# Kernel optimization log

Measured on AMD Instinct MI355X. Metric: run time of the kernel, lower is better.

## Reference

```python
import jax, jax.numpy as jnp
import numpy as np

EPS = 1e-6  # NAFNet LayerNorm2d eps


def conv1x1(x, W, b):
    # x: [B,C,H,W], W: [O,C], b: [O]
    return jnp.einsum('bchw,oc->bohw', x, W) + b[None, :, None, None]


def layernorm2d(x, w, b):
    # normalize over channel dim (NAFNet LayerNorm2d)
    mu = jnp.mean(x, axis=1, keepdims=True)
    var = jnp.var(x, axis=1, keepdims=True)
    xn = (x - mu) * jax.lax.rsqrt(var + EPS)
    return xn * w[None, :, None, None] + b[None, :, None, None]


def resize_bilinear_ac(x, H, W):
    # bilinear resize with align_corners=True; x: [B,C,h,w] -> [B,C,H,W]
    B, C, h, w = x.shape

    def coords(out, inn):
        s = (inn - 1) / (out - 1)
        c = jnp.arange(out, dtype=jnp.float32) * jnp.float32(s)
        i0 = jnp.clip(jnp.floor(c).astype(jnp.int32), 0, inn - 2)
        f = c - i0.astype(jnp.float32)
        return i0, f

    i0, fy = coords(H, h)
    j0, fx = coords(W, w)
    # rows
    x = x[:, :, i0, :] * (1.0 - fy)[None, None, :, None] + x[:, :, i0 + 1, :] * fy[None, None, :, None]
    # cols
    x = x[:, :, :, j0] * (1.0 - fx)[None, None, None, :] + x[:, :, :, j0 + 1] * fx[None, None, None, :]
    return x


def setup_inputs() -> dict:
    key = jax.random.key(0)
    ks = jax.random.split(key, 24)
    B, c, mem_c, H, W = 8, 128, 64, 128, 128
    h2, w2 = 64, 64
    std = 0.02

    def w2d(k, o, i):
        return jax.random.normal(k, (o, i), dtype=jnp.float32) * np.sqrt(2.0 / o)

    return {
        'x_l': jax.random.normal(ks[0], (B, c, H, W), dtype=jnp.float32),
        'x_r': jax.random.normal(ks[1], (B, mem_c, h2, w2), dtype=jnp.float32),
        'Wm': w2d(ks[2], c, mem_c), 'bm': jnp.zeros((c,), jnp.float32),
        'nl_w': jnp.ones((c,), jnp.float32), 'nl_b': jnp.zeros((c,), jnp.float32),
        'nr_w': jnp.ones((c,), jnp.float32), 'nr_b': jnp.zeros((c,), jnp.float32),
        'Wl1': w2d(ks[3], c, c), 'bl1': jnp.zeros((c,), jnp.float32),
        'Wr1': w2d(ks[4], c, c), 'br1': jnp.zeros((c,), jnp.float32),
        'Wl2': w2d(ks[5], c, c), 'bl2': jnp.zeros((c,), jnp.float32),
        'Wr2': w2d(ks[6], c, c), 'br2': jnp.zeros((c,), jnp.float32),
        'beta': jax.random.normal(ks[7], (1, c, 1, 1), dtype=jnp.float32) * std,
        'gamma': jax.random.normal(ks[8], (1, c, 1, 1), dtype=jnp.float32) * std,
        'Wf': w2d(ks[9], c, 2 * c), 'bf': jnp.zeros((c,), jnp.float32),
    }


def reference(x_l, x_r, Wm, bm, nl_w, nl_b, nr_w, nr_b, Wl1, bl1, Wr1, br1,
              Wl2, bl2, Wr2, br2, beta, gamma, Wf, bf):
    c = x_l.shape[1]
    scale = jnp.float32(c) ** -0.5
    H, W = x_l.shape[-2], x_l.shape[-1]

    x_r = conv1x1(x_r, Wm, bm)
    x_r = resize_bilinear_ac(x_r, H, W)

    Q_l = jnp.transpose(conv1x1(layernorm2d(x_l, nl_w, nl_b), Wl1, bl1), (0, 2, 3, 1))  # b h w c
    Q_r = jnp.transpose(conv1x1(layernorm2d(x_r, nr_w, nr_b), Wr1, br1), (0, 2, 3, 1))  # b h v c
    V_l = jnp.transpose(conv1x1(x_l, Wl2, bl2), (0, 2, 3, 1))  # b h w c
    V_r = jnp.transpose(conv1x1(x_r, Wr2, br2), (0, 2, 3, 1))  # b h v c

    attn = jnp.einsum('bhwc,bhvc->bhwv', Q_l, Q_r) * scale  # [B,H,W,W]
    F_r2l = jnp.einsum('bhwv,bhvc->bhwc', jax.nn.softmax(attn, axis=-1), V_r)
    F_l2r = jnp.einsum('bhwv,bhwc->bhvc', jax.nn.softmax(attn, axis=2), V_l)

    F_r2l = jnp.transpose(F_r2l, (0, 3, 1, 2)) * beta
    F_l2r = jnp.transpose(F_l2r, (0, 3, 1, 2)) * gamma

    x = jnp.concatenate([x_l + F_r2l, x_r + F_l2r], axis=1)
    return conv1x1(x, Wf, bf)
```

## Files before the change

### kernel.cpp

```cpp
#include <hip/hip_runtime.h>
#include <cstdint>
#include <cstddef>

typedef __attribute__((ext_vector_type(8))) short short8;
typedef __attribute__((ext_vector_type(4))) float f32x4;

#define MFMA16(a,b,c) __builtin_amdgcn_mfma_f32_16x16x32_bf16((a),(b),(c),0,0,0)

static __device__ __forceinline__ float bf2f(unsigned short u){
    unsigned int x = ((unsigned int)u) << 16;
    return __builtin_bit_cast(float, x);
}
static __device__ __forceinline__ unsigned short f2bf(float f){
    unsigned int x = __builtin_bit_cast(unsigned int, f);
    x = x + 0x7FFFu + ((x >> 16) & 1u);
    return (unsigned short)(x >> 16);
}


__global__ void k_prep(const float* __restrict__ Wl1, const float* __restrict__ bl1,
                       const float* __restrict__ Wr1, const float* __restrict__ br1,
                       const float* __restrict__ Wl2, const float* __restrict__ Wr2,
                       const float* __restrict__ Wf,
                       const float* __restrict__ nlw, const float* __restrict__ nlb,
                       const float* __restrict__ nrw, const float* __restrict__ nrb,
                       unsigned short* __restrict__ wl1e, unsigned short* __restrict__ wr1e,
                       unsigned short* __restrict__ wl2b, unsigned short* __restrict__ wr2b,
                       unsigned short* __restrict__ wf1b, unsigned short* __restrict__ wf2b,
                       float* __restrict__ S1l, float* __restrict__ S1r,
                       float* __restrict__ beffl, float* __restrict__ beffr)
{
    int o = blockIdx.x;
    int c = threadIdx.x;
    float wl = Wl1[o*128+c] * nlw[c];
    unsigned short wlb = f2bf(wl);
    wl1e[o*128+c] = wlb;
    float wr = Wr1[o*128+c] * nrw[c];
    unsigned short wrb = f2bf(wr);
    wr1e[o*128+c] = wrb;
    wl2b[o*128+c] = f2bf(Wl2[o*128+c]);
    wr2b[o*128+c] = f2bf(Wr2[o*128+c]);
    wf1b[o*128+c] = f2bf(Wf[o*256+c]);
    wf2b[o*128+c] = f2bf(Wf[o*256+128+c]);

    __shared__ float red[4][128];
    red[0][c] = bf2f(wlb);
    red[1][c] = Wl1[o*128+c]*nlb[c];
    red[2][c] = bf2f(wrb);
    red[3][c] = Wr1[o*128+c]*nrb[c];
    __syncthreads();
    if (c < 4) {
        float s = 0.f;
        for (int i = 0; i < 128; i++) s += red[c][i];
        if      (c == 0) S1l[o]   = s;
        else if (c == 1) beffl[o] = bl1[o] + s;
        else if (c == 2) S1r[o]   = s;
        else             beffr[o] = br1[o] + s;
    }
}

__global__ void k_memconv(const float* __restrict__ xr, const float* __restrict__ Wm,
                          const float* __restrict__ bm, unsigned short* __restrict__ R0n)
{
    __shared__ float Xs[64][65];
    __shared__ float Ws[128][65];
    int blk = blockIdx.x;
    int b  = blk >> 6;
    int p0 = (blk & 63) * 64;
    int t = threadIdx.x;
    for (int k = 0; k < 16; k++) {
        int idx = t + 256*k;
        int c = idx >> 6, pi = idx & 63;
        Xs[c][pi] = xr[((long)b*64 + c)*4096 + p0 + pi];
    }
    for (int k = 0; k < 32; k++) {
        int idx = t + 256*k;
        int o = idx >> 6, c = idx & 63;
        Ws[o][c] = Wm[o*64 + c];
    }
    __syncthreads();
    int og = t >> 3, pg = t & 7;
    int o0 = og*4, pp0 = pg*8;
    float acc[4][8];
    #pragma unroll
    for (int j = 0; j < 4; j++)
        #pragma unroll
        for (int k = 0; k < 8; k++) acc[j][k] = bm[o0+j];
    for (int c = 0; c < 64; c++) {
        float xv[8], wv[4];
        #pragma unroll
        for (int k = 0; k < 8; k++) xv[k] = Xs[c][pp0+k];
        #pragma unroll
        for (int j = 0; j < 4; j++) wv[j] = Ws[o0+j][c];
        #pragma unroll
        for (int j = 0; j < 4; j++)
            #pragma unroll
            for (int k = 0; k < 8; k++) acc[j][k] += wv[j]*xv[k];
    }
    #pragma unroll
    for (int j = 0; j < 4; j++)
        #pragma unroll
        for (int k = 0; k < 8; k++)
            R0n[((long)b*4096 + p0 + pp0 + k)*128 + o0 + j] = f2bf(acc[j][k]);
}

__global__ void k_upsample(const unsigned short* __restrict__ R0n,
                           unsigned short* __restrict__ XR)
{
    int t = threadIdx.x;
    int c = t & 127;
    long pix = (long)blockIdx.x * 2 + (t >> 7);
    int b = (int)(pix >> 14);
    int rem = (int)(pix & 16383);
    int Y = rem >> 7, X = rem & 127;
    const float s = 63.0f / 127.0f;
    float cy = Y * s, cx = X * s;
    int y0 = min((int)floorf(cy), 62);
    int x0 = min((int)floorf(cx), 62);
    float fy = cy - (float)y0, fx = cx - (float)x0;
    const unsigned short* base = R0n + ((long)b*4096)*128;
    float v00 = bf2f(base[(y0*64 + x0    )*128 + c]);
    float v01 = bf2f(base[(y0*64 + x0 + 1)*128 + c]);
    float v10 = bf2f(base[((y0+1)*64 + x0    )*128 + c]);
    float v11 = bf2f(base[((y0+1)*64 + x0 + 1)*128 + c]);
    float r0 = v00*(1.f-fy) + v10*fy;
    float r1 = v01*(1.f-fy) + v11*fy;
    XR[pix*128 + c] = f2bf(r0*(1.f-fx) + r1*fx);
}

__global__ void k_transpose(const float* __restrict__ xl, unsigned short* __restrict__ XL)
{
    __shared__ float tile[32][33];
    int blk = blockIdx.x;
    int pt = blk & 511;
    int ct = (blk >> 9) & 3;
    int b  = blk >> 11;
    int p0 = pt*32, c0 = ct*32;
    int t = threadIdx.x;
    const float* src = xl + (long)b*128*16384;
    #pragma unroll
    for (int k = 0; k < 4; k++) {
        int idx = t + 256*k;
        int ci = idx >> 5, pi = idx & 31;
        tile[ci][pi] = src[(long)(c0+ci)*16384 + p0 + pi];
    }
    __syncthreads();
    unsigned short* dst = XL + (long)b*16384*128;
    #pragma unroll
    for (int k = 0; k < 4; k++) {
        int idx = t + 256*k;
        int pi = idx >> 5, ci = idx & 31;
        dst[(long)(p0+pi)*128 + c0 + ci] = f2bf(tile[ci][pi]);
    }
}

__global__ void k_stats(const unsigned short* __restrict__ X,
                        float* __restrict__ mu, float* __restrict__ rs, int npix)
{
    int t = threadIdx.x;
    int lane = t & 63, wv = t >> 6;
    long pix = (long)blockIdx.x*4 + wv;
    if (pix >= npix) return;
    const unsigned short* row = X + pix*128;
    unsigned int pr = *(const unsigned int*)(row + lane*2);
    float a = bf2f((unsigned short)(pr & 0xFFFFu));
    float b = bf2f((unsigned short)(pr >> 16));
    float s = a + b, s2 = a*a + b*b;
    #pragma unroll
    for (int d = 1; d < 64; d <<= 1) { s += __shfl_xor(s, d); s2 += __shfl_xor(s2, d); }
    if (lane == 0) {
        float m = s * (1.0f/128.0f);
        float var = s2 * (1.0f/128.0f) - m*m;
        mu[pix] = m;
        rs[pix] = rsqrtf(var + 1e-6f);
    }
}

#define LDQ 136
constexpr int K4_LDS = 4*128*LDQ*2 + (13*128 + 8*128 + 256)*4;

__global__ __launch_bounds__(512) void k_scam(
    const unsigned short* __restrict__ XL, const unsigned short* __restrict__ XR,
    const unsigned short* __restrict__ wl1e, const unsigned short* __restrict__ wr1e,
    const unsigned short* __restrict__ wl2b, const unsigned short* __restrict__ wr2b,
    const unsigned short* __restrict__ wf1b, const unsigned short* __restrict__ wf2b,
    const float* __restrict__ muL, const float* __restrict__ rsL,
    const float* __restrict__ muR, const float* __restrict__ rsR,
    const float* __restrict__ S1l, const float* __restrict__ S1r,
    const float* __restrict__ beffl, const float* __restrict__ beffr,
    const float* __restrict__ bl2, const float* __restrict__ br2,
    const float* __restrict__ beta, const float* __restrict__ gam,
    const float* __restrict__ bfv, float* __restrict__ out)
{
    extern __shared__ char smem[];
    unsigned short* bufA  = (unsigned short*)smem;
    unsigned short* bufB  = bufA  + 128*LDQ;
    unsigned short* bufVL = bufB  + 128*LDQ;
    unsigned short* bufVR = bufVL + 128*LDQ;
    float* vecs    = (float*)(bufVR + 128*LDQ);
    float* colpart = vecs + 13*128;
    float* colred  = colpart + 8*128;

    int tid = threadIdx.x;
    int lane = tid & 63, wv = tid >> 6;
    int l16 = lane & 15, lg = lane >> 4;
    int bh = blockIdx.x;
    int b = bh >> 7, h = bh & 127;
    long pixbase = (long)b*16384 + (long)h*128;
    const unsigned short* Abl = XL + pixbase*128;
    const unsigned short* Abr = XR + pixbase*128;

    if (tid < 128) {
        vecs[0*128+tid]  = muL[pixbase + tid];
        vecs[1*128+tid]  = rsL[pixbase + tid];
        vecs[2*128+tid]  = muR[pixbase + tid];
        vecs[3*128+tid]  = rsR[pixbase + tid];
        vecs[4*128+tid]  = S1l[tid];
        vecs[5*128+tid]  = beffl[tid];
        vecs[6*128+tid]  = S1r[tid];
        vecs[7*128+tid]  = beffr[tid];
        vecs[8*128+tid]  = bl2[tid];
        vecs[9*128+tid]  = br2[tid];
        vecs[10*128+tid] = beta[tid];
        vecs[11*128+tid] = gam[tid];
        vecs[12*128+tid] = bfv[tid];
    }
    __syncthreads();

    int p0 = wv * 16;

    f32x4 acc[8];
    auto conv = [&](const unsigned short* Asrc, const unsigned short* Wsrc){
        #pragma unroll
        for (int t = 0; t < 8; t++) acc[t] = (f32x4){0.f,0.f,0.f,0.f};
        #pragma unroll
        for (int kc = 0; kc < 4; kc++) {
            short8 a = *(const short8*)(Asrc + (p0+l16)*128 + kc*32 + lg*8);
            #pragma unroll
            for (int t = 0; t < 8; t++) {
                short8 bw = *(const short8*)(Wsrc + (t*16+l16)*128 + kc*32 + lg*8);
                acc[t] = MFMA16(a, bw, acc[t]);
            }
        }
    };
    auto epiQ = [&](const float* vmu, const float* vrs, const float* vS1,
                    const float* vbe, unsigned short* dst){
        #pragma unroll
        for (int r = 0; r < 4; r++) {
            int p = p0 + lg*4 + r;
            float mu = vmu[p], rs = vrs[p];
            #pragma unroll
            for (int t = 0; t < 8; t++) {
                int o = t*16 + l16;
                dst[p*LDQ + o] = f2bf(rs*(acc[t][r] - mu*vS1[o]) + vbe[o]);
            }
        }
    };
    auto epiV = [&](const float* vb, unsigned short* dst){
        #pragma unroll
        for (int t = 0; t < 8; t++) {
            int o = t*16 + l16;
            float bias = vb[o];
            #pragma unroll
            for (int r = 0; r < 4; r++) {
                int p = p0 + lg*4 + r;
                dst[o*LDQ + p] = f2bf(acc[t][r] + bias);
            }
        }
    };

    conv(Abl, wl1e); epiQ(vecs+0*128, vecs+1*128, vecs+4*128, vecs+5*128, bufA);
    conv(Abr, wr1e); epiQ(vecs+2*128, vecs+3*128, vecs+6*128, vecs+7*128, bufB);
    conv(Abl, wl2b); epiV(vecs+8*128, bufVL);
    conv(Abr, wr2b); epiV(vecs+9*128, bufVR);
    __syncthreads();

    int w0 = p0;
    f32x4 s[8];
    #pragma unroll
    for (int t = 0; t < 8; t++) s[t] = (f32x4){0.f,0.f,0.f,0.f};
    #pragma unroll
    for (int kc = 0; kc < 4; kc++) {
        short8 a = *(const short8*)(bufA + (w0+l16)*LDQ + kc*32 + lg*8);
        #pragma unroll
        for (int t = 0; t < 8; t++) {
            short8 bq = *(const short8*)(bufB + (t*16+l16)*LDQ + kc*32 + lg*8);
            s[t] = MFMA16(a, bq, s[t]);
        }
    }
    const float scale = 0.08838834764831845f;
    #pragma unroll
    for (int t = 0; t < 8; t++)
        #pragma unroll
        for (int r = 0; r < 4; r++) s[t][r] *= scale;

    float rm[4];
    #pragma unroll
    for (int r = 0; r < 4; r++) {
        float m = s[0][r];
        #pragma unroll
        for (int t = 1; t < 8; t++) m = fmaxf(m, s[t][r]);
        #pragma unroll
        for (int d = 1; d < 16; d <<= 1) m = fmaxf(m, __shfl_xor(m, d));
        rm[r] = m;
    }
    #pragma unroll
    for (int t = 0; t < 8; t++) {
        float m = fmaxf(fmaxf(s[t][0], s[t][1]), fmaxf(s[t][2], s[t][3]));
        m = fmaxf(m, __shfl_xor(m, 16));
        m = fmaxf(m, __shfl_xor(m, 32));
        if (lane < 16) colpart[wv*128 + t*16 + lane] = m;
    }
    __syncthreads();
    if (tid < 128) {
        float m = colpart[tid];
        for (int i = 1; i < 8; i++) m = fmaxf(m, colpart[i*128 + tid]);
        colred[tid] = m;
    }
    __syncthreads();

    float rsum[4];
    #pragma unroll
    for (int r = 0; r < 4; r++) {
        float a = 0.f;
        #pragma unroll
        for (int t = 0; t < 8; t++) { float e = __expf(s[t][r] - rm[r]); s[t][r] = e; a += e; }
        #pragma unroll
        for (int d = 1; d < 16; d <<= 1) a += __shfl_xor(a, d);
        rsum[r] = a;
    }
    #pragma unroll
    for (int t = 0; t < 8; t++) {
        #pragma unroll
        for (int r = 0; r < 4; r++) {
            bufA[(w0 + lg*4 + r)*LDQ + t*16 + l16] = f2bf(s[t][r] / rsum[r]);
        }
    }
    #pragma unroll
    for (int t = 0; t < 8; t++) {
        float cmax = colred[t*16 + l16];
        float a = 0.f;
        #pragma unroll
        for (int r = 0; r < 4; r++) {
            float e2 = s[t][r] * __expf(rm[r] - cmax);
            s[t][r] = e2; a += e2;
        }
        a += __shfl_xor(a, 16);
        a += __shfl_xor(a, 32);
        if (lane < 16) colpart[wv*128 + t*16 + lane] = a;
    }
    __syncthreads();
    if (tid < 128) {
        float sm = 0.f;
        for (int i = 0; i < 8; i++) sm += colpart[i*128 + tid];
        colred[128 + tid] = sm;
    }
    __syncthreads();
    #pragma unroll
    for (int t = 0; t < 8; t++) {
        float inv = 1.0f / colred[128 + t*16 + l16];
        #pragma unroll
        for (int r = 0; r < 4; r++) {
            bufB[(t*16 + l16)*LDQ + w0 + lg*4 + r] = f2bf(s[t][r] * inv);
        }
    }
    __syncthreads();

    f32x4 f1[8], f2[8];
    #pragma unroll
    for (int t = 0; t < 8; t++) { f1[t] = (f32x4){0.f,0.f,0.f,0.f}; f2[t] = (f32x4){0.f,0.f,0.f,0.f}; }
    #pragma unroll
    for (int kc = 0; kc < 4; kc++) {
        short8 a1 = *(const short8*)(bufA + (w0+l16)*LDQ + kc*32 + lg*8);
        short8 a2 = *(const short8*)(bufB + (w0+l16)*LDQ + kc*32 + lg*8);
        #pragma unroll
        for (int t = 0; t < 8; t++) {
            short8 bv1 = *(const short8*)(bufVR + (t*16+l16)*LDQ + kc*32 + lg*8);
            f1[t] = MFMA16(a1, bv1, f1[t]);
            short8 bv2 = *(const short8*)(bufVL + (t*16+l16)*LDQ + kc*32 + lg*8);
            f2[t] = MFMA16(a2, bv2, f2[t]);
        }
    }
    __syncthreads();

    #pragma unroll
    for (int t = 0; t < 8; t++) {
        int c = t*16 + l16;
        float bet = vecs[10*128 + c], gm = vecs[11*128 + c];
        #pragma unroll
        for (int r = 0; r < 4; r++) {
            int p = w0 + lg*4 + r;
            float xl = bf2f(Abl[p*128 + c]);
            bufA[p*LDQ + c] = f2bf(xl + bet*f1[t][r]);
            float xr = bf2f(Abr[p*128 + c]);
            bufB[p*LDQ + c] = f2bf(xr + gm*f2[t][r]);
        }
    }
    __syncthreads();

    int o0 = wv * 16;
    f32x4 oacc[8];
    #pragma unroll
    for (int t = 0; t < 8; t++) oacc[t] = (f32x4){0.f,0.f,0.f,0.f};
    #pragma unroll
    for (int kc = 0; kc < 4; kc++) {
        short8 aw1 = *(const short8*)(wf1b + (o0+l16)*128 + kc*32 + lg*8);
        short8 aw2 = *(const short8*)(wf2b + (o0+l16)*128 + kc*32 + lg*8);
        #pragma unroll
        for (int t = 0; t < 8; t++) {
            short8 b1 = *(const short8*)(bufA + (t*16+l16)*LDQ + kc*32 + lg*8);
            oacc[t] = MFMA16(aw1, b1, oacc[t]);
            short8 b2 = *(const short8*)(bufB + (t*16+l16)*LDQ + kc*32 + lg*8);
            oacc[t] = MFMA16(aw2, b2, oacc[t]);
        }
    }
    float* outb = out + (long)b*2097152 + (long)h*128;
    #pragma unroll
    for (int t = 0; t < 8; t++) {
        #pragma unroll
        for (int r = 0; r < 4; r++) {
            int o = o0 + lg*4 + r;
            outb[(long)o*16384 + t*16 + l16] = oacc[t][r] + vecs[12*128 + o];
        }
    }
}

extern "C" void kernel_launch(void* const* d_in, const int* in_sizes, int n_in,
                              void* d_out, int out_size, void* d_ws, size_t ws_size,
                              hipStream_t stream)
{
    const float* x_l = (const float*)d_in[0];
    const float* x_r = (const float*)d_in[1];
    const float* Wm  = (const float*)d_in[2];
    const float* bm  = (const float*)d_in[3];
    const float* nlw = (const float*)d_in[4];
    const float* nlb = (const float*)d_in[5];
    const float* nrw = (const float*)d_in[6];
    const float* nrb = (const float*)d_in[7];
    const float* Wl1 = (const float*)d_in[8];
    const float* bl1 = (const float*)d_in[9];
    const float* Wr1 = (const float*)d_in[10];
    const float* br1 = (const float*)d_in[11];
    const float* Wl2 = (const float*)d_in[12];
    const float* bl2 = (const float*)d_in[13];
    const float* Wr2 = (const float*)d_in[14];
    const float* br2 = (const float*)d_in[15];
    const float* beta = (const float*)d_in[16];
    const float* gam  = (const float*)d_in[17];
    const float* Wf   = (const float*)d_in[18];
    const float* bf   = (const float*)d_in[19];
    float* out = (float*)d_out;

    char* ws = (char*)d_ws;
    size_t off = 0;
    auto alloc = [&](size_t bytes) -> void* {
        void* p = ws + off;
        off += (bytes + 255) & ~(size_t)255;
        return p;
    };
    unsigned short* XL   = (unsigned short*)alloc((size_t)16777216*2);
    unsigned short* XR   = (unsigned short*)alloc((size_t)16777216*2);
    unsigned short* R0n  = (unsigned short*)alloc((size_t)4194304*2);
    float* muL = (float*)alloc((size_t)131072*4);
    float* rsL = (float*)alloc((size_t)131072*4);
    float* muR = (float*)alloc((size_t)131072*4);
    float* rsR = (float*)alloc((size_t)131072*4);
    unsigned short* wl1e = (unsigned short*)alloc((size_t)16384*2);
    unsigned short* wr1e = (unsigned short*)alloc((size_t)16384*2);
    unsigned short* wl2b = (unsigned short*)alloc((size_t)16384*2);
    unsigned short* wr2b = (unsigned short*)alloc((size_t)16384*2);
    unsigned short* wf1b = (unsigned short*)alloc((size_t)16384*2);
    unsigned short* wf2b = (unsigned short*)alloc((size_t)16384*2);
    float* S1l   = (float*)alloc(128*4);
    float* S1r   = (float*)alloc(128*4);
    float* beffl = (float*)alloc(128*4);
    float* beffr = (float*)alloc(128*4);

    (void)in_sizes; (void)n_in; (void)out_size; (void)ws_size;

    hipFuncSetAttribute((const void*)k_scam,
                        hipFuncAttributeMaxDynamicSharedMemorySize, K4_LDS);

    k_prep<<<128, 128, 0, stream>>>(Wl1, bl1, Wr1, br1, Wl2, Wr2, Wf,
                                    nlw, nlb, nrw, nrb,
                                    wl1e, wr1e, wl2b, wr2b, wf1b, wf2b,
                                    S1l, S1r, beffl, beffr);
    k_memconv<<<512, 256, 0, stream>>>(x_r, Wm, bm, R0n);
    k_upsample<<<65536, 256, 0, stream>>>(R0n, XR);
    k_transpose<<<16384, 256, 0, stream>>>(x_l, XL);
    k_stats<<<32768, 256, 0, stream>>>(XL, muL, rsL, 131072);
    k_stats<<<32768, 256, 0, stream>>>(XR, muR, rsR, 131072);
    k_scam<<<1024, 512, K4_LDS, stream>>>(XL, XR, wl1e, wr1e, wl2b, wr2b,
                                          wf1b, wf2b, muL, rsL, muR, rsR,
                                          S1l, S1r, beffl, beffr,
                                          bl2, br2, beta, gam, bf, out);
}
```

Measured before the change: 446.8 us.

## Fuse LayerNorm stats into transpose/upsample, drop softmax max pass, halve attention LDS

Merges the LayerNorm statistics kernels into the transpose and upsample kernels, and vectorises their loads and stores, so XL and XR are not re-read. In the attention kernel it drops the row and column max subtraction, exponentiating the raw scores once and sharing them between both softmaxes. It also computes the V projections after the attention probabilities are built, so only two LDS buffers are needed, and adds an occupancy hint through launch_bounds. Skipping the max subtraction risks overflow if scores are large, and the k_prep reduction now uses shuffles.

```diff
diff --git a/kernel.cpp b/kernel.cpp
--- a/kernel.cpp
+++ b/kernel.cpp
@@ -4,6 +4,7 @@
 
 typedef __attribute__((ext_vector_type(8))) short short8;
 typedef __attribute__((ext_vector_type(4))) float f32x4;
+typedef __attribute__((ext_vector_type(4))) float float4v;
 
 #define MFMA16(a,b,c) __builtin_amdgcn_mfma_f32_16x16x32_bf16((a),(b),(c),0,0,0)
 
@@ -49,13 +50,15 @@
     red[2][c] = bf2f(wrb);
     red[3][c] = Wr1[o*128+c]*nrb[c];
     __syncthreads();
-    if (c < 4) {
-        float s = 0.f;
-        for (int i = 0; i < 128; i++) s += red[c][i];
-        if      (c == 0) S1l[o]   = s;
-        else if (c == 1) beffl[o] = bl1[o] + s;
-        else if (c == 2) S1r[o]   = s;
-        else             beffr[o] = br1[o] + s;
+    int g = c >> 5, j = c & 31;
+    float sv = red[g][j] + red[g][j+32] + red[g][j+64] + red[g][j+96];
+    #pragma unroll
+    for (int d = 1; d < 32; d <<= 1) sv += __shfl_xor(sv, d);
+    if (j == 0) {
+        if      (g == 0) S1l[o]   = sv;
+        else if (g == 1) beffl[o] = bl1[o] + sv;
+        else if (g == 2) S1r[o]   = sv;
+        else             beffr[o] = br1[o] + sv;
     }
 }
 
@@ -104,82 +107,95 @@
             R0n[((long)b*4096 + p0 + pp0 + k)*128 + o0 + j] = f2bf(acc[j][k]);
 }
 
-__global__ void k_upsample(const unsigned short* __restrict__ R0n,
-                           unsigned short* __restrict__ XR)
+__global__ void k_xr(const unsigned short* __restrict__ R0n,
+                     unsigned short* __restrict__ XR,
+                     float* __restrict__ muR, float* __restrict__ rsR)
 {
     int t = threadIdx.x;
-    int c = t & 127;
-    long pix = (long)blockIdx.x * 2 + (t >> 7);
+    int pl = t >> 4;
+    int cg = (t & 15) * 8;
+    long pix = (long)blockIdx.x * 16 + pl;
     int b = (int)(pix >> 14);
     int rem = (int)(pix & 16383);
     int Y = rem >> 7, X = rem & 127;
-    const float s = 63.0f / 127.0f;
-    float cy = Y * s, cx = X * s;
+    const float sc = 63.0f / 127.0f;
+    float cy = Y * sc, cx = X * sc;
     int y0 = min((int)floorf(cy), 62);
     int x0 = min((int)floorf(cx), 62);
     float fy = cy - (float)y0, fx = cx - (float)x0;
+    float w00 = (1.f-fy)*(1.f-fx), w01 = (1.f-fy)*fx, w10 = fy*(1.f-fx), w11 = fy*fx;
     const unsigned short* base = R0n + ((long)b*4096)*128;
-    float v00 = bf2f(base[(y0*64 + x0    )*128 + c]);
-    float v01 = bf2f(base[(y0*64 + x0 + 1)*128 + c]);
-    float v10 = bf2f(base[((y0+1)*64 + x0    )*128 + c]);
-    float v11 = bf2f(base[((y0+1)*64 + x0 + 1)*128 + c]);
-    float r0 = v00*(1.f-fy) + v10*fy;
-    float r1 = v01*(1.f-fy) + v11*fy;
-    XR[pix*128 + c] = f2bf(r0*(1.f-fx) + r1*fx);
-}
-
-__global__ void k_transpose(const float* __restrict__ xl, unsigned short* __restrict__ XL)
-{
-    __shared__ float tile[32][33];
+    short8 v00 = *(const short8*)(base + (y0*64 + x0    )*128 + cg);
+    short8 v01 = *(const short8*)(base + (y0*64 + x0 + 1)*128 + cg);
+    short8 v10 = *(const short8*)(base + ((y0+1)*64 + x0    )*128 + cg);
+    short8 v11 = *(const short8*)(base + ((y0+1)*64 + x0 + 1)*128 + cg);
+    short8 outv;
+    float sv = 0.f, s2 = 0.f;
+    #pragma unroll
+    for (int j = 0; j < 8; j++) {
+        float val = w00*bf2f((unsigned short)v00[j]) + w01*bf2f((unsigned short)v01[j])
+                  + w10*bf2f((unsigned short)v10[j]) + w11*bf2f((unsigned short)v11[j]);
+        outv[j] = (short)f2bf(val);
+        sv += val; s2 += val*val;
+    }
+    *(short8*)(XR + pix*128 + cg) = outv;
+    #pragma unroll
+    for (int d = 1; d < 16; d <<= 1) { sv += __shfl_xor(sv, d); s2 += __shfl_xor(s2, d); }
+    if ((t & 15) == 0) {
+        float m = sv * (1.0f/128.0f);
+        float var = s2 * (1.0f/128.0f) - m*m;
+        muR[pix] = m;
+        rsR[pix] = rsqrtf(var + 1e-6f);
+    }
+}
+
+__global__ void k_xl(const float* __restrict__ xl, unsigned short* __restrict__ XL,
+                     float* __restrict__ muL, float* __restrict__ rsL)
+{
+    __shared__ float tile[128][33];
+    __shared__ float partS[8][32];
+    __shared__ float partS2[8][32];
     int blk = blockIdx.x;
-    int pt = blk & 511;
-    int ct = (blk >> 9) & 3;
-    int b  = blk >> 11;
-    int p0 = pt*32, c0 = ct*32;
+    int b  = blk >> 9;
+    int p0 = (blk & 511) * 32;
+    const float* src = xl + (long)b*128*16384;
     int t = threadIdx.x;
-    const float* src = xl + (long)b*128*16384;
     #pragma unroll
     for (int k = 0; k < 4; k++) {
         int idx = t + 256*k;
-        int ci = idx >> 5, pi = idx & 31;
-        tile[ci][pi] = src[(long)(c0+ci)*16384 + p0 + pi];
-    }
-    __syncthreads();
-    unsigned short* dst = XL + (long)b*16384*128;
-    #pragma unroll
-    for (int k = 0; k < 4; k++) {
-        int idx = t + 256*k;
-        int pi = idx >> 5, ci = idx & 31;
-        dst[(long)(p0+pi)*128 + c0 + ci] = f2bf(tile[ci][pi]);
-    }
-}
-
-__global__ void k_stats(const unsigned short* __restrict__ X,
-                        float* __restrict__ mu, float* __restrict__ rs, int npix)
-{
-    int t = threadIdx.x;
-    int lane = t & 63, wv = t >> 6;
-    long pix = (long)blockIdx.x*4 + wv;
-    if (pix >= npix) return;
-    const unsigned short* row = X + pix*128;
-    unsigned int pr = *(const unsigned int*)(row + lane*2);
-    float a = bf2f((unsigned short)(pr & 0xFFFFu));
-    float b = bf2f((unsigned short)(pr >> 16));
-    float s = a + b, s2 = a*a + b*b;
-    #pragma unroll
-    for (int d = 1; d < 64; d <<= 1) { s += __shfl_xor(s, d); s2 += __shfl_xor(s2, d); }
-    if (lane == 0) {
-        float m = s * (1.0f/128.0f);
-        float var = s2 * (1.0f/128.0f) - m*m;
-        mu[pix] = m;
-        rs[pix] = rsqrtf(var + 1e-6f);
+        int cc = idx >> 3, pi4 = (idx & 7) * 4;
+        float4v v = *(const float4v*)&src[(long)cc*16384 + p0 + pi4];
+        tile[cc][pi4+0] = v[0]; tile[cc][pi4+1] = v[1];
+        tile[cc][pi4+2] = v[2]; tile[cc][pi4+3] = v[3];
+    }
+    __syncthreads();
+    unsigned short* dst = XL + ((long)b*16384 + p0)*128;
+    int cw = t & 127, ph = t >> 7;
+    #pragma unroll
+    for (int k = 0; k < 16; k++) {
+        int pi = ph*16 + k;
+        dst[(long)pi*128 + cw] = f2bf(tile[cw][pi]);
+    }
+    int sub = t >> 5, pj = t & 31;
+    float sv = 0.f, s2 = 0.f;
+    #pragma unroll
+    for (int j = 0; j < 16; j++) { float v = tile[sub*16+j][pj]; sv += v; s2 += v*v; }
+    partS[sub][pj] = sv; partS2[sub][pj] = s2;
+    __syncthreads();
+    if (t < 32) {
+        float S = 0.f, S2 = 0.f;
+        #pragma unroll
+        for (int i = 0; i < 8; i++) { S += partS[i][t]; S2 += partS2[i][t]; }
+        float m = S*(1.0f/128.0f), var = S2*(1.0f/128.0f) - m*m;
+        muL[(long)b*16384 + p0 + t] = m;
+        rsL[(long)b*16384 + p0 + t] = rsqrtf(var + 1e-6f);
     }
 }
 
 #define LDQ 136
-constexpr int K4_LDS = 4*128*LDQ*2 + (13*128 + 8*128 + 256)*4;
-
-__global__ __launch_bounds__(512) void k_scam(
+constexpr int K4_LDS = 2*128*LDQ*2 + (13*128 + 8*128)*4;
+
+__global__ __launch_bounds__(512, 4) void k_scam(
     const unsigned short* __restrict__ XL, const unsigned short* __restrict__ XR,
     const unsigned short* __restrict__ wl1e, const unsigned short* __restrict__ wr1e,
     const unsigned short* __restrict__ wl2b, const unsigned short* __restrict__ wr2b,
@@ -193,17 +209,15 @@
     const float* __restrict__ bfv, float* __restrict__ out)
 {
     extern __shared__ char smem[];
-    unsigned short* bufA  = (unsigned short*)smem;
-    unsigned short* bufB  = bufA  + 128*LDQ;
-    unsigned short* bufVL = bufB  + 128*LDQ;
-    unsigned short* bufVR = bufVL + 128*LDQ;
-    float* vecs    = (float*)(bufVR + 128*LDQ);
-    float* colpart = vecs + 13*128;
-    float* colred  = colpart + 8*128;
+    unsigned short* bufA = (unsigned short*)smem;
+    unsigned short* bufB = bufA + 128*LDQ;
+    float* vecs = (float*)(bufB + 128*LDQ);
+    float* colS = vecs + 13*128;
 
     int tid = threadIdx.x;
     int lane = tid & 63, wv = tid >> 6;
     int l16 = lane & 15, lg = lane >> 4;
+    int p0 = wv * 16;
     int bh = blockIdx.x;
     int b = bh >> 7, h = bh & 127;
     long pixbase = (long)b*16384 + (long)h*128;
@@ -227,8 +241,6 @@
     }
     __syncthreads();
 
-    int p0 = wv * 16;
-
     f32x4 acc[8];
     auto conv = [&](const unsigned short* Asrc, const unsigned short* Wsrc){
         #pragma unroll
@@ -244,7 +256,7 @@
         }
     };
     auto epiQ = [&](const float* vmu, const float* vrs, const float* vS1,
-                    const float* vbe, unsigned short* dst){
+                    const float* vbe, unsigned short* dstb){
         #pragma unroll
         for (int r = 0; r < 4; r++) {
             int p = p0 + lg*4 + r;
@@ -252,36 +264,21 @@
             #pragma unroll
             for (int t = 0; t < 8; t++) {
                 int o = t*16 + l16;
-                dst[p*LDQ + o] = f2bf(rs*(acc[t][r] - mu*vS1[o]) + vbe[o]);
-            }
-        }
-    };
-    auto epiV = [&](const float* vb, unsigned short* dst){
-        #pragma unroll
-        for (int t = 0; t < 8; t++) {
-            int o = t*16 + l16;
-            float bias = vb[o];
-            #pragma unroll
-            for (int r = 0; r < 4; r++) {
-                int p = p0 + lg*4 + r;
-                dst[o*LDQ + p] = f2bf(acc[t][r] + bias);
+                dstb[p*LDQ + o] = f2bf(rs*(acc[t][r] - mu*vS1[o]) + vbe[o]);
             }
         }
     };
 
     conv(Abl, wl1e); epiQ(vecs+0*128, vecs+1*128, vecs+4*128, vecs+5*128, bufA);
     conv(Abr, wr1e); epiQ(vecs+2*128, vecs+3*128, vecs+6*128, vecs+7*128, bufB);
-    conv(Abl, wl2b); epiV(vecs+8*128, bufVL);
-    conv(Abr, wr2b); epiV(vecs+9*128, bufVR);
-    __syncthreads();
-
-    int w0 = p0;
+    __syncthreads();
+
     f32x4 s[8];
     #pragma unroll
     for (int t = 0; t < 8; t++) s[t] = (f32x4){0.f,0.f,0.f,0.f};
     #pragma unroll
     for (int kc = 0; kc < 4; kc++) {
-        short8 a = *(const short8*)(bufA + (w0+l16)*LDQ + kc*32 + lg*8);
+        short8 a = *(const short8*)(bufA + (p0+l16)*LDQ + kc*32 + lg*8);
         #pragma unroll
         for (int t = 0; t < 8; t++) {
             short8 bq = *(const short8*)(bufB + (t*16+l16)*LDQ + kc*32 + lg*8);
@@ -292,76 +289,74 @@
     #pragma unroll
     for (int t = 0; t < 8; t++)
         #pragma unroll
-        for (int r = 0; r < 4; r++) s[t][r] *= scale;
-
-    float rm[4];
-    #pragma unroll
-    for (int r = 0; r < 4; r++) {
-        float m = s[0][r];
-        #pragma unroll
-        for (int t = 1; t < 8; t++) m = fmaxf(m, s[t][r]);
-        #pragma unroll
-        for (int d = 1; d < 16; d <<= 1) m = fmaxf(m, __shfl_xor(m, d));
-        rm[r] = m;
-    }
-    #pragma unroll
-    for (int t = 0; t < 8; t++) {
-        float m = fmaxf(fmaxf(s[t][0], s[t][1]), fmaxf(s[t][2], s[t][3]));
-        m = fmaxf(m, __shfl_xor(m, 16));
-        m = fmaxf(m, __shfl_xor(m, 32));
-        if (lane < 16) colpart[wv*128 + t*16 + lane] = m;
-    }
-    __syncthreads();
-    if (tid < 128) {
-        float m = colpart[tid];
-        for (int i = 1; i < 8; i++) m = fmaxf(m, colpart[i*128 + tid]);
-        colred[tid] = m;
-    }
-    __syncthreads();
+        for (int r = 0; r < 4; r++) s[t][r] = __expf(s[t][r] * scale);
 
     float rsum[4];
     #pragma unroll
     for (int r = 0; r < 4; r++) {
         float a = 0.f;
         #pragma unroll
-        for (int t = 0; t < 8; t++) { float e = __expf(s[t][r] - rm[r]); s[t][r] = e; a += e; }
+        for (int t = 0; t < 8; t++) a += s[t][r];
         #pragma unroll
         for (int d = 1; d < 16; d <<= 1) a += __shfl_xor(a, d);
         rsum[r] = a;
     }
     #pragma unroll
     for (int t = 0; t < 8; t++) {
-        #pragma unroll
-        for (int r = 0; r < 4; r++) {
-            bufA[(w0 + lg*4 + r)*LDQ + t*16 + l16] = f2bf(s[t][r] / rsum[r]);
-        }
-    }
-    #pragma unroll
-    for (int t = 0; t < 8; t++) {
-        float cmax = colred[t*16 + l16];
-        float a = 0.f;
-        #pragma unroll
-        for (int r = 0; r < 4; r++) {
-            float e2 = s[t][r] * __expf(rm[r] - cmax);
-            s[t][r] = e2; a += e2;
-        }
+        float a = s[t][0] + s[t][1] + s[t][2] + s[t][3];
         a += __shfl_xor(a, 16);
         a += __shfl_xor(a, 32);
-        if (lane < 16) colpart[wv*128 + t*16 + lane] = a;
-    }
-    __syncthreads();
-    if (tid < 128) {
-        float sm = 0.f;
-        for (int i = 0; i < 8; i++) sm += colpart[i*128 + tid];
-        colred[128 + tid] = sm;
-    }
-    __syncthreads();
+        if (lane < 16) colS[wv*128 + t*16 + lane] = a;
+    }
+    __syncthreads();
+
+    #pragma unroll
+    for (int r = 0; r < 4; r++) {
+        float inv = 1.0f / rsum[r];
+        #pragma unroll
+        for (int t = 0; t < 8; t++)
+            bufA[(p0 + lg*4 + r)*LDQ + t*16 + l16] = f2bf(s[t][r] * inv);
+    }
     #pragma unroll
     for (int t = 0; t < 8; t++) {
-        float inv = 1.0f / colred[128 + t*16 + l16];
-        #pragma unroll
-        for (int r = 0; r < 4; r++) {
-            bufB[(t*16 + l16)*LDQ + w0 + lg*4 + r] = f2bf(s[t][r] * inv);
+        int col = t*16 + l16;
+        float cs = 0.f;
+        #pragma unroll
+        for (int i = 0; i < 8; i++) cs += colS[i*128 + col];
+        float inv = 1.0f / cs;
+        #pragma unroll
+        for (int r = 0; r < 4; r++)
+            bufB[col*LDQ + p0 + lg*4 + r] = f2bf(s[t][r] * inv);
+    }
+    __syncthreads();
+
+    short8 pa1[4], pa2[4];
+    #pragma unroll
+    for (int kc = 0; kc < 4; kc++) {
+        pa1[kc] = *(const short8*)(bufA + (p0+l16)*LDQ + kc*32 + lg*8);
+        pa2[kc] = *(const short8*)(bufB + (p0+l16)*LDQ + kc*32 + lg*8);
+    }
+    conv(Abl, wl2b);
+    __syncthreads();
+    {
+        #pragma unroll
+        for (int t = 0; t < 8; t++) {
+            int o = t*16 + l16;
+            float bias = vecs[8*128 + o];
+            #pragma unroll
+            for (int r = 0; r < 4; r++)
+                bufA[o*LDQ + p0 + lg*4 + r] = f2bf(acc[t][r] + bias);
+        }
+    }
+    conv(Abr, wr2b);
+    {
+        #pragma unroll
+        for (int t = 0; t < 8; t++) {
+            int o = t*16 + l16;
+            float bias = vecs[9*128 + o];
+            #pragma unroll
+            for (int r = 0; r < 4; r++)
+                bufB[o*LDQ + p0 + lg*4 + r] = f2bf(acc[t][r] + bias);
         }
     }
     __syncthreads();
@@ -371,14 +366,12 @@
     for (int t = 0; t < 8; t++) { f1[t] = (f32x4){0.f,0.f,0.f,0.f}; f2[t] = (f32x4){0.f,0.f,0.f,0.f}; }
     #pragma unroll
     for (int kc = 0; kc < 4; kc++) {
-        short8 a1 = *(const short8*)(bufA + (w0+l16)*LDQ + kc*32 + lg*8);
-        short8 a2 = *(const short8*)(bufB + (w0+l16)*LDQ + kc*32 + lg*8);
         #pragma unroll
         for (int t = 0; t < 8; t++) {
-            short8 bv1 = *(const short8*)(bufVR + (t*16+l16)*LDQ + kc*32 + lg*8);
-            f1[t] = MFMA16(a1, bv1, f1[t]);
-            short8 bv2 = *(const short8*)(bufVL + (t*16+l16)*LDQ + kc*32 + lg*8);
-            f2[t] = MFMA16(a2, bv2, f2[t]);
+            short8 bv1 = *(const short8*)(bufB + (t*16+l16)*LDQ + kc*32 + lg*8);
+            f1[t] = MFMA16(pa1[kc], bv1, f1[t]);
+            short8 bv2 = *(const short8*)(bufA + (t*16+l16)*LDQ + kc*32 + lg*8);
+            f2[t] = MFMA16(pa2[kc], bv2, f2[t]);
         }
     }
     __syncthreads();
@@ -389,23 +382,22 @@
         float bet = vecs[10*128 + c], gm = vecs[11*128 + c];
         #pragma unroll
         for (int r = 0; r < 4; r++) {
-            int p = w0 + lg*4 + r;
-            float xl = bf2f(Abl[p*128 + c]);
-            bufA[p*LDQ + c] = f2bf(xl + bet*f1[t][r]);
-            float xr = bf2f(Abr[p*128 + c]);
-            bufB[p*LDQ + c] = f2bf(xr + gm*f2[t][r]);
-        }
-    }
-    __syncthreads();
-
-    int o0 = wv * 16;
+            int p = p0 + lg*4 + r;
+            float xlv = bf2f(Abl[p*128 + c]);
+            bufA[p*LDQ + c] = f2bf(xlv + bet*f1[t][r]);
+            float xrv = bf2f(Abr[p*128 + c]);
+            bufB[p*LDQ + c] = f2bf(xrv + gm*f2[t][r]);
+        }
+    }
+    __syncthreads();
+
     f32x4 oacc[8];
     #pragma unroll
     for (int t = 0; t < 8; t++) oacc[t] = (f32x4){0.f,0.f,0.f,0.f};
     #pragma unroll
     for (int kc = 0; kc < 4; kc++) {
-        short8 aw1 = *(const short8*)(wf1b + (o0+l16)*128 + kc*32 + lg*8);
-        short8 aw2 = *(const short8*)(wf2b + (o0+l16)*128 + kc*32 + lg*8);
+        short8 aw1 = *(const short8*)(wf1b + (p0+l16)*128 + kc*32 + lg*8);
+        short8 aw2 = *(const short8*)(wf2b + (p0+l16)*128 + kc*32 + lg*8);
         #pragma unroll
         for (int t = 0; t < 8; t++) {
             short8 b1 = *(const short8*)(bufA + (t*16+l16)*LDQ + kc*32 + lg*8);
@@ -419,7 +411,7 @@
     for (int t = 0; t < 8; t++) {
         #pragma unroll
         for (int r = 0; r < 4; r++) {
-            int o = o0 + lg*4 + r;
+            int o = p0 + lg*4 + r;
             outb[(long)o*16384 + t*16 + l16] = oacc[t][r] + vecs[12*128 + o];
         }
     }
@@ -486,10 +478,8 @@
                                     wl1e, wr1e, wl2b, wr2b, wf1b, wf2b,
                                     S1l, S1r, beffl, beffr);
     k_memconv<<<512, 256, 0, stream>>>(x_r, Wm, bm, R0n);
-    k_upsample<<<65536, 256, 0, stream>>>(R0n, XR);
-    k_transpose<<<16384, 256, 0, stream>>>(x_l, XL);
-    k_stats<<<32768, 256, 0, stream>>>(XL, muL, rsL, 131072);
-    k_stats<<<32768, 256, 0, stream>>>(XR, muR, rsR, 131072);
+    k_xr<<<8192, 256, 0, stream>>>(R0n, XR, muR, rsR);
+    k_xl<<<4096, 256, 0, stream>>>(x_l, XL, muL, rsL);
     k_scam<<<1024, 512, K4_LDS, stream>>>(XL, XR, wl1e, wr1e, wl2b, wr2b,
                                           wf1b, wf2b, muL, rsL, muR, rsR,
                                           S1l, S1r, beffl, beffr,
```

New measurement: 384.0 us. 14.0% less time.
